# Optimization experiments

Hardware: AMD Instinct MI355X
Metric: run time of the kernel (lower is better)

## Reference

```python
import jax, jax.numpy as jnp
import numpy as np

B, S, D = 4, 4096, 2048
NUM_MODALITIES = 2


def setup_inputs() -> dict:
    key = jax.random.key(0)
    k_x, k_t, k_w0, k_b0, k_w1, k_b1 = jax.random.split(key, 6)
    scale = 1.0 / np.sqrt(D)
    return {
        "hidden_states": jax.random.normal(k_x, (B, S, D), dtype=jnp.float32),
        "type_ids": jax.random.randint(k_t, (B, S), 0, NUM_MODALITIES, dtype=jnp.int32),
        "W0": jax.random.uniform(k_w0, (D, D), jnp.float32, -scale, scale),
        "b0": jax.random.uniform(k_b0, (D,), jnp.float32, -scale, scale),
        "W1": jax.random.uniform(k_w1, (D, D), jnp.float32, -scale, scale),
        "b1": jax.random.uniform(k_b1, (D,), jnp.float32, -scale, scale),
    }


def reference(hidden_states, type_ids, W0, b0, W1, b1):
    # Original: gather tokens where type_ids == i, apply expert i's Linear,
    # scatter into a zero-init [B, S, out_dim] buffer. The masks partition
    # all tokens, so this equals a masked mixture of the two dense GEMMs.
    y0 = jnp.einsum("bsd,ed->bse", hidden_states, W0) + b0  # expert 0
    y1 = jnp.einsum("bsd,ed->bse", hidden_states, W1) + b1  # expert 1
    m0 = (type_ids == 0)[..., None]
    m1 = (type_ids == 1)[..., None]
    zero = jnp.zeros((), dtype=y0.dtype)
    return jnp.where(m0, y0, zero) + jnp.where(m1, y1, zero)
```

## Files before the change

### kernel.cpp

```cpp
#include <hip/hip_runtime.h>
#include <hip/hip_bf16.h>
#include <stdint.h>


#define T_TOK 16384
#define DDIM  2048
#define NT_K  32
#define MT    64
#define NTILE 8

typedef __attribute__((ext_vector_type(4))) float          f32x4;
typedef __attribute__((ext_vector_type(8))) short          bf16x8;
typedef __attribute__((ext_vector_type(2))) unsigned int   u32x2;

#define WS_HBF   0ull
#define WS_W0BF  67108864ull
#define WS_W1BF  75497472ull
#define WS_META  83886080ull
#define WS_IDX   83886208ull
#define WS_NEED  (WS_IDX + 65536ull)

__device__ __forceinline__ unsigned short cvt1_bf16(float f) {
  unsigned u = __builtin_bit_cast(unsigned, f);
  unsigned rnd = 0x7fffu + ((u >> 16) & 1u);
  return (unsigned short)((u + rnd) >> 16);
}

__device__ __forceinline__ void gload_lds16(const void* g, void* l) {
  __builtin_amdgcn_global_load_lds(
      (const __attribute__((address_space(1))) unsigned int*)g,
      (__attribute__((address_space(3))) unsigned int*)l, 16, 0, 0);
}

#define BAR()    asm volatile("s_barrier" ::: "memory")
#define VMCNT4() asm volatile("s_waitcnt vmcnt(4)" ::: "memory")
#define VMCNT0() asm volatile("s_waitcnt vmcnt(0)" ::: "memory")
#define LGKM0()  asm volatile("s_waitcnt lgkmcnt(0)" ::: "memory")

__global__ void k_prep(const float* __restrict__ H, const float* __restrict__ W0,
                       const float* __restrict__ W1, const int* __restrict__ typ,
                       unsigned short* __restrict__ Hbf,
                       unsigned short* __restrict__ W0bf,
                       unsigned short* __restrict__ W1bf,
                       int* __restrict__ meta) {
  const int gid = blockIdx.x * blockDim.x + threadIdx.x;
  if (gid < T_TOK && typ[gid] == 0) atomicAdd(&meta[0], 1);
  const int nH = T_TOK * DDIM / 4;
  const int nW = DDIM * DDIM / 4;
  const int total = nH + 2 * nW;
  const int stride = gridDim.x * blockDim.x;
  for (int i = gid; i < total; i += stride) {
    const float* s; unsigned short* d; int j;
    if (i < nH)           { s = H;  d = Hbf;  j = i; }
    else if (i < nH + nW) { s = W0; d = W0bf; j = i - nH; }
    else                  { s = W1; d = W1bf; j = i - nH - nW; }
    f32x4 v = ((const f32x4*)s)[j];
    unsigned p0 = (unsigned)cvt1_bf16(v[0]) | ((unsigned)cvt1_bf16(v[1]) << 16);
    unsigned p1 = (unsigned)cvt1_bf16(v[2]) | ((unsigned)cvt1_bf16(v[3]) << 16);
    u32x2 o; o[0] = p0; o[1] = p1;
    ((u32x2*)d)[j] = o;
  }
}

__global__ void k_scatter(const int* __restrict__ typ, int* __restrict__ meta,
                          int* __restrict__ idx) {
  int i = blockIdx.x * blockDim.x + threadIdx.x;
  if (i >= T_TOK) return;
  int c0 = meta[0];
  int t = typ[i];
  int pos = (t == 0) ? atomicAdd(&meta[2], 1) : c0 + atomicAdd(&meta[3], 1);
  idx[pos] = i;
}

__global__ __launch_bounds__(512, 2) void k_gemm256(
    const unsigned short* __restrict__ Hbf,
    const unsigned short* __restrict__ W0bf,
    const unsigned short* __restrict__ W1bf,
    const float* __restrict__ B0, const float* __restrict__ B1,
    const int* __restrict__ meta, const int* __restrict__ idx,
    float* __restrict__ OUT)
{
  __shared__ char lds[131072];

  const int orig = blockIdx.x;
  const int wg = (orig & 7) * 64 + (orig >> 3);
  const int my = wg >> 3;
  const int bx = wg & 7;

  const int tid  = threadIdx.x;
  const int lane = tid & 63;
  const int wid  = tid >> 6;
  const int wr   = wid >> 2;
  const int wc   = wid & 3;
  const int fr   = lane & 15;
  const int g    = lane >> 4;

  const int start = my * 256;
  const int c0    = meta[0];
  const int e0    = (start >= c0) ? 1 : 0;
  const int e1    = (start < c0 && c0 < start + 256) ? 1 : e0;
  const int colBase = bx * 256;

  const int cs = (lane & 3) ^ ((lane >> 3) & 3);
  const char* aS[2];
  int rt[2];
#pragma unroll
  for (int l = 0; l < 2; ++l) {
    int ch = 2 * wid + l;
    rt[l] = ch * 16 + (lane >> 2);
    int orow = idx[start + rt[l]];
    aS[l] = (const char*)Hbf + (size_t)orow * 4096 + cs * 16;
  }
  const int chB = (2 * wid) * 1024;

  const int sw = (g ^ ((fr >> 1) & 3)) << 4;
  int aF[8], bF[4];
#pragma unroll
  for (int m = 0; m < 8; ++m) aF[m] = ((wr * 128 + m * 16 + fr) << 6) + sw;
#pragma unroll
  for (int n = 0; n < 4; ++n) bF[n] = ((wc * 64 + n * 16 + fr) << 6) + sw;

  for (int e = e0; e <= e1; ++e) {
    const unsigned short* Wb = e ? W1bf : W0bf;
    const char* wS[2];
#pragma unroll
    for (int l = 0; l < 2; ++l)
      wS[l] = (const char*)(Wb + (size_t)(colBase + rt[l]) * DDIM) + cs * 16;

    f32x4 acc[8][4];
#pragma unroll
    for (int m = 0; m < 8; ++m)
#pragma unroll
      for (int n = 0; n < 4; ++n) acc[m][n] = (f32x4)0.0f;

    auto STAGE_A = [&](int d, int kh, int tn) {
      char* dst = lds + (d << 15) + (kh << 14) + chB;
      int ko = tn * 128 + kh * 64;
      gload_lds16(aS[0] + ko, dst);
      gload_lds16(aS[1] + ko, dst + 1024);
    };
    auto STAGE_B = [&](int d, int kh, int tn) {
      char* dst = lds + 65536 + (d << 15) + (kh << 14) + chB;
      int ko = tn * 128 + kh * 64;
      gload_lds16(wS[0] + ko, dst);
      gload_lds16(wS[1] + ko, dst + 1024);
    };

    VMCNT0();
    BAR();

    STAGE_A(0, 0, 0); STAGE_B(0, 0, 0); STAGE_A(0, 1, 0); STAGE_B(0, 1, 0);
    VMCNT4();
    BAR();

#pragma unroll 2
    for (int t = 0; t < NT_K; ++t) {
      const int c = t & 1, d = c ^ 1;
      int tn = t + 1; if (tn == NT_K) tn = NT_K - 1;
      const char* Ak0 = lds + (c << 15);
      const char* Ak1 = Ak0 + 16384;
      const char* Bk0 = lds + 65536 + (c << 15);
      const char* Bk1 = Bk0 + 16384;

      bf16x8 a[8], b0v, b1v, b2v, b3v;

#pragma unroll
      for (int m = 0; m < 8; ++m) a[m] = *(const bf16x8*)(Ak0 + aF[m]);
      b0v = *(const bf16x8*)(Bk0 + bF[0]);
      b1v = *(const bf16x8*)(Bk0 + bF[1]);
      STAGE_A(d, 0, tn);
      BAR(); LGKM0();
      __builtin_amdgcn_s_setprio(1);
#pragma unroll
      for (int m = 0; m < 8; ++m) {
        acc[m][0] = __builtin_amdgcn_mfma_f32_16x16x32_bf16(a[m], b0v, acc[m][0], 0, 0, 0);
        acc[m][1] = __builtin_amdgcn_mfma_f32_16x16x32_bf16(a[m], b1v, acc[m][1], 0, 0, 0);
      }
      __builtin_amdgcn_s_setprio(0);
      BAR();

      b2v = *(const bf16x8*)(Bk0 + bF[2]);
      b3v = *(const bf16x8*)(Bk0 + bF[3]);
      STAGE_B(d, 0, tn);
      VMCNT4();
      BAR(); LGKM0();
      __builtin_amdgcn_s_setprio(1);
#pragma unroll
      for (int m = 0; m < 8; ++m) {
        acc[m][2] = __builtin_amdgcn_mfma_f32_16x16x32_bf16(a[m], b2v, acc[m][2], 0, 0, 0);
        acc[m][3] = __builtin_amdgcn_mfma_f32_16x16x32_bf16(a[m], b3v, acc[m][3], 0, 0, 0);
      }
      __builtin_amdgcn_s_setprio(0);
      BAR();

#pragma unroll
      for (int m = 0; m < 8; ++m) a[m] = *(const bf16x8*)(Ak1 + aF[m]);
      b0v = *(const bf16x8*)(Bk1 + bF[0]);
      b1v = *(const bf16x8*)(Bk1 + bF[1]);
      STAGE_A(d, 1, tn);
      BAR(); LGKM0();
      __builtin_amdgcn_s_setprio(1);
#pragma unroll
      for (int m = 0; m < 8; ++m) {
        acc[m][0] = __builtin_amdgcn_mfma_f32_16x16x32_bf16(a[m], b0v, acc[m][0], 0, 0, 0);
        acc[m][1] = __builtin_amdgcn_mfma_f32_16x16x32_bf16(a[m], b1v, acc[m][1], 0, 0, 0);
      }
      __builtin_amdgcn_s_setprio(0);
      BAR();

      b2v = *(const bf16x8*)(Bk1 + bF[2]);
      b3v = *(const bf16x8*)(Bk1 + bF[3]);
      STAGE_B(d, 1, tn);
      VMCNT4();
      BAR(); LGKM0();
      __builtin_amdgcn_s_setprio(1);
#pragma unroll
      for (int m = 0; m < 8; ++m) {
        acc[m][2] = __builtin_amdgcn_mfma_f32_16x16x32_bf16(a[m], b2v, acc[m][2], 0, 0, 0);
        acc[m][3] = __builtin_amdgcn_mfma_f32_16x16x32_bf16(a[m], b3v, acc[m][3], 0, 0, 0);
      }
      __builtin_amdgcn_s_setprio(0);
      BAR();
    }

    const float* Bv = e ? B1 : B0;
    float bias[4];
    int cols[4];
#pragma unroll
    for (int n = 0; n < 4; ++n) {
      cols[n] = colBase + wc * 64 + n * 16 + fr;
      bias[n] = Bv[cols[n]];
    }
#pragma unroll
    for (int m = 0; m < 8; ++m) {
      int lb = wr * 128 + m * 16 + (g << 2);
#pragma unroll
      for (int j = 0; j < 4; ++j) {
        int p = start + lb + j;
        if (((p >= c0) ? 1 : 0) != e) continue;
        int orow = idx[p];
        float* op = OUT + (size_t)orow * DDIM;
#pragma unroll
        for (int n = 0; n < 4; ++n) op[cols[n]] = acc[m][n][j] + bias[n];
      }
    }
  }
}

#define BMd 64
#define BNd 64
#define BKd 32
#define LDW 36

__device__ __forceinline__ bf16x8 cvt_bf16x8(f32x4 lo, f32x4 hi) {
  bf16x8 r;
#pragma unroll
  for (int i = 0; i < 4; ++i) {
    r[i]     = (short)cvt1_bf16(lo[i]);
    r[i + 4] = (short)cvt1_bf16(hi[i]);
  }
  return r;
}

__global__ __launch_bounds__(256, 2) void mot_mfma_diag(
    const float* __restrict__ H,  const int* __restrict__ TYP,
    const float* __restrict__ W0, const float* __restrict__ B0,
    const float* __restrict__ W1, const float* __restrict__ B1,
    float* __restrict__ OUT)
{
  __shared__ float As[BMd * LDW];
  __shared__ float W0s[BNd * LDW];
  __shared__ float W1s[BNd * LDW];

  const int tid = threadIdx.x;
  const int rowBase = blockIdx.y * BMd;
  const int colBase = blockIdx.x * BNd;
  const int srow  = tid >> 3;
  const int scol4 = (tid & 7) << 2;
  const float* hA  = H  + (size_t)(rowBase + srow) * DDIM + scol4;
  const float* hW0 = W0 + (size_t)(colBase + srow) * DDIM + scol4;
  const float* hW1 = W1 + (size_t)(colBase + srow) * DDIM + scol4;

  const int lane = tid & 63;
  const int w    = tid >> 6;
  const int fr   = lane & 15;
  const int g    = lane >> 4;

  f32x4 acc0[4], acc1[4];
#pragma unroll
  for (int m = 0; m < 4; ++m) { acc0[m] = (f32x4)0.0f; acc1[m] = (f32x4)0.0f; }

  for (int k0 = 0; k0 < DDIM; k0 += BKd) {
    f32x4 va[2], v0[2], v1[2];
#pragma unroll
    for (int p = 0; p < 2; ++p) {
      va[p] = *(const f32x4*)(hA  + (size_t)p * 32 * DDIM);
      v0[p] = *(const f32x4*)(hW0 + (size_t)p * 32 * DDIM);
      v1[p] = *(const f32x4*)(hW1 + (size_t)p * 32 * DDIM);
    }
    hA += BKd; hW0 += BKd; hW1 += BKd;
    __syncthreads();
#pragma unroll
    for (int p = 0; p < 2; ++p) {
      int r = srow + 32 * p;
      *(f32x4*)(&As [r * LDW + scol4]) = va[p];
      *(f32x4*)(&W0s[r * LDW + scol4]) = v0[p];
      *(f32x4*)(&W1s[r * LDW + scol4]) = v1[p];
    }
    __syncthreads();

    bf16x8 af[4];
#pragma unroll
    for (int m = 0; m < 4; ++m) {
      const float* ap = &As[(m * 16 + fr) * LDW + g * 8];
      af[m] = cvt_bf16x8(*(const f32x4*)ap, *(const f32x4*)(ap + 4));
    }
    const float* b0p = &W0s[(w * 16 + fr) * LDW + g * 8];
    const float* b1p = &W1s[(w * 16 + fr) * LDW + g * 8];
    bf16x8 bf0 = cvt_bf16x8(*(const f32x4*)b0p, *(const f32x4*)(b0p + 4));
    bf16x8 bf1 = cvt_bf16x8(*(const f32x4*)b1p, *(const f32x4*)(b1p + 4));
#pragma unroll
    for (int m = 0; m < 4; ++m) {
      acc0[m] = __builtin_amdgcn_mfma_f32_16x16x32_bf16(af[m], bf0, acc0[m], 0, 0, 0);
      acc1[m] = __builtin_amdgcn_mfma_f32_16x16x32_bf16(af[m], bf1, acc1[m], 0, 0, 0);
    }
  }

  const int col = colBase + w * 16 + fr;
  const float bz0 = B0[col];
  const float bz1 = B1[col];
#pragma unroll
  for (int m = 0; m < 4; ++m)
#pragma unroll
    for (int j = 0; j < 4; ++j) {
      int row = rowBase + m * 16 + (g << 2) + j;
      int t = TYP[row];
      OUT[(size_t)row * DDIM + col] = (t == 0) ? (acc0[m][j] + bz0) : (acc1[m][j] + bz1);
    }
}

extern "C" void kernel_launch(void* const* d_in, const int* in_sizes, int n_in,
                              void* d_out, int out_size, void* d_ws, size_t ws_size,
                              hipStream_t stream) {
  const float* H   = (const float*)d_in[0];
  const int*   TYP = (const int*)  d_in[1];
  const float* W0  = (const float*)d_in[2];
  const float* B0v = (const float*)d_in[3];
  const float* W1  = (const float*)d_in[4];
  const float* B1v = (const float*)d_in[5];
  float* OUT = (float*)d_out;

  if (ws_size < WS_NEED) {
    dim3 grid(DDIM / BNd, T_TOK / BMd);
    mot_mfma_diag<<<grid, dim3(256), 0, stream>>>(H, TYP, W0, B0v, W1, B1v, OUT);
    return;
  }

  unsigned short* Hbf  = (unsigned short*)((char*)d_ws + WS_HBF);
  unsigned short* W0bf = (unsigned short*)((char*)d_ws + WS_W0BF);
  unsigned short* W1bf = (unsigned short*)((char*)d_ws + WS_W1BF);
  int* meta = (int*)((char*)d_ws + WS_META);
  int* idx  = (int*)((char*)d_ws + WS_IDX);

  hipMemsetAsync(meta, 0, 16, stream);
  k_prep   <<<4096, 256, 0, stream>>>(H, W0, W1, TYP, Hbf, W0bf, W1bf, meta);
  k_scatter<<<64,   256, 0, stream>>>(TYP, meta, idx);
  k_gemm256<<<MT * NTILE, 512, 0, stream>>>(Hbf, W0bf, W1bf, B0v, B1v, meta, idx, OUT);
}
```

Baseline: 238.0 us.

## Deepen GEMM prefetch pipeline and schedule mixed-expert row tile first

The main loop now prefetches global-to-LDS loads two k-steps ahead instead of one, reusing freed half-buffers within the current slot, and relaxes the vmcnt waits to allow more loads in flight. The per-phase register tiling moves from 8 A-fragments x 2 B-fragments to 4 A x 4 B, which changes how fragments are reused. The row tile that straddles the expert boundary (and needs both experts) is swapped into block slot zero so the heavier tile starts early. This aims to hide memory latency and reduce tail imbalance, at the cost of more complex buffer-reuse ordering that must stay race-free.

```diff
diff --git a/kernel.cpp b/kernel.cpp
--- a/kernel.cpp
+++ b/kernel.cpp
@@ -32,10 +32,10 @@
       (__attribute__((address_space(3))) unsigned int*)l, 16, 0, 0);
 }
 
-#define BAR()    asm volatile("s_barrier" ::: "memory")
-#define VMCNT4() asm volatile("s_waitcnt vmcnt(4)" ::: "memory")
-#define VMCNT0() asm volatile("s_waitcnt vmcnt(0)" ::: "memory")
-#define LGKM0()  asm volatile("s_waitcnt lgkmcnt(0)" ::: "memory")
+#define BAR()     asm volatile("s_barrier" ::: "memory")
+#define VMCNT10() asm volatile("s_waitcnt vmcnt(10)" ::: "memory")
+#define VMCNT0()  asm volatile("s_waitcnt vmcnt(0)" ::: "memory")
+#define LGKM0()   asm volatile("s_waitcnt lgkmcnt(0)" ::: "memory")
 
 __global__ void k_prep(const float* __restrict__ H, const float* __restrict__ W0,
                        const float* __restrict__ W1, const int* __restrict__ typ,
@@ -84,8 +84,12 @@
 
   const int orig = blockIdx.x;
   const int wg = (orig & 7) * 64 + (orig >> 3);
-  const int my = wg >> 3;
+  int my = wg >> 3;
   const int bx = wg & 7;
+
+  const int c0 = meta[0];
+  int ms = c0 >> 8; if (ms > MT - 1) ms = MT - 1;
+  my = (my == 0) ? ms : (my == ms) ? 0 : my;
 
   const int tid  = threadIdx.x;
   const int lane = tid & 63;
@@ -96,7 +100,6 @@
   const int g    = lane >> 4;
 
   const int start = my * 256;
-  const int c0    = meta[0];
   const int e0    = (start >= c0) ? 1 : 0;
   const int e1    = (start < c0 && c0 < start + 256) ? 1 : e0;
   const int colBase = bx * 256;
@@ -149,76 +152,80 @@
     VMCNT0();
     BAR();
 
-    STAGE_A(0, 0, 0); STAGE_B(0, 0, 0); STAGE_A(0, 1, 0); STAGE_B(0, 1, 0);
-    VMCNT4();
+    STAGE_B(0, 0, 0); STAGE_A(0, 0, 0);
+    STAGE_B(0, 1, 0); STAGE_A(0, 1, 0);
+    STAGE_B(1, 0, 1); STAGE_A(1, 0, 1);
+    STAGE_B(1, 1, 1);
+    VMCNT10();
     BAR();
 
 #pragma unroll 2
     for (int t = 0; t < NT_K; ++t) {
       const int c = t & 1, d = c ^ 1;
-      int tn = t + 1; if (tn == NT_K) tn = NT_K - 1;
+      int t1 = t + 1; if (t1 >= NT_K) t1 = NT_K - 1;
+      int t2 = t + 2; if (t2 >= NT_K) t2 = NT_K - 1;
       const char* Ak0 = lds + (c << 15);
       const char* Ak1 = Ak0 + 16384;
       const char* Bk0 = lds + 65536 + (c << 15);
       const char* Bk1 = Bk0 + 16384;
 
-      bf16x8 a[8], b0v, b1v, b2v, b3v;
-
-#pragma unroll
-      for (int m = 0; m < 8; ++m) a[m] = *(const bf16x8*)(Ak0 + aF[m]);
-      b0v = *(const bf16x8*)(Bk0 + bF[0]);
-      b1v = *(const bf16x8*)(Bk0 + bF[1]);
-      STAGE_A(d, 0, tn);
+      bf16x8 a[4], b[4];
+
+#pragma unroll
+      for (int m = 0; m < 4; ++m) a[m] = *(const bf16x8*)(Ak0 + aF[m]);
+#pragma unroll
+      for (int n = 0; n < 4; ++n) b[n] = *(const bf16x8*)(Bk0 + bF[n]);
+      STAGE_A(d, 1, t1);
       BAR(); LGKM0();
       __builtin_amdgcn_s_setprio(1);
 #pragma unroll
-      for (int m = 0; m < 8; ++m) {
-        acc[m][0] = __builtin_amdgcn_mfma_f32_16x16x32_bf16(a[m], b0v, acc[m][0], 0, 0, 0);
-        acc[m][1] = __builtin_amdgcn_mfma_f32_16x16x32_bf16(a[m], b1v, acc[m][1], 0, 0, 0);
-      }
+      for (int n = 0; n < 4; ++n)
+#pragma unroll
+        for (int m = 0; m < 4; ++m)
+          acc[m][n] = __builtin_amdgcn_mfma_f32_16x16x32_bf16(a[m], b[n], acc[m][n], 0, 0, 0);
       __builtin_amdgcn_s_setprio(0);
       BAR();
 
-      b2v = *(const bf16x8*)(Bk0 + bF[2]);
-      b3v = *(const bf16x8*)(Bk0 + bF[3]);
-      STAGE_B(d, 0, tn);
-      VMCNT4();
+#pragma unroll
+      for (int m = 0; m < 4; ++m) a[m] = *(const bf16x8*)(Ak0 + aF[m + 4]);
+      STAGE_B(c, 0, t2);
+      VMCNT10();
       BAR(); LGKM0();
       __builtin_amdgcn_s_setprio(1);
 #pragma unroll
-      for (int m = 0; m < 8; ++m) {
-        acc[m][2] = __builtin_amdgcn_mfma_f32_16x16x32_bf16(a[m], b2v, acc[m][2], 0, 0, 0);
-        acc[m][3] = __builtin_amdgcn_mfma_f32_16x16x32_bf16(a[m], b3v, acc[m][3], 0, 0, 0);
-      }
+      for (int n = 0; n < 4; ++n)
+#pragma unroll
+        for (int m = 0; m < 4; ++m)
+          acc[m + 4][n] = __builtin_amdgcn_mfma_f32_16x16x32_bf16(a[m], b[n], acc[m + 4][n], 0, 0, 0);
       __builtin_amdgcn_s_setprio(0);
       BAR();
 
 #pragma unroll
-      for (int m = 0; m < 8; ++m) a[m] = *(const bf16x8*)(Ak1 + aF[m]);
-      b0v = *(const bf16x8*)(Bk1 + bF[0]);
-      b1v = *(const bf16x8*)(Bk1 + bF[1]);
-      STAGE_A(d, 1, tn);
+      for (int m = 0; m < 4; ++m) a[m] = *(const bf16x8*)(Ak1 + aF[m]);
+#pragma unroll
+      for (int n = 0; n < 4; ++n) b[n] = *(const bf16x8*)(Bk1 + bF[n]);
+      STAGE_A(c, 0, t2);
       BAR(); LGKM0();
       __builtin_amdgcn_s_setprio(1);
 #pragma unroll
-      for (int m = 0; m < 8; ++m) {
-        acc[m][0] = __builtin_amdgcn_mfma_f32_16x16x32_bf16(a[m], b0v, acc[m][0], 0, 0, 0);
-        acc[m][1] = __builtin_amdgcn_mfma_f32_16x16x32_bf16(a[m], b1v, acc[m][1], 0, 0, 0);
-      }
+      for (int n = 0; n < 4; ++n)
+#pragma unroll
+        for (int m = 0; m < 4; ++m)
+          acc[m][n] = __builtin_amdgcn_mfma_f32_16x16x32_bf16(a[m], b[n], acc[m][n], 0, 0, 0);
       __builtin_amdgcn_s_setprio(0);
       BAR();
 
-      b2v = *(const bf16x8*)(Bk1 + bF[2]);
-      b3v = *(const bf16x8*)(Bk1 + bF[3]);
-      STAGE_B(d, 1, tn);
-      VMCNT4();
+#pragma unroll
+      for (int m = 0; m < 4; ++m) a[m] = *(const bf16x8*)(Ak1 + aF[m + 4]);
+      STAGE_B(c, 1, t2);
+      VMCNT10();
       BAR(); LGKM0();
       __builtin_amdgcn_s_setprio(1);
 #pragma unroll
-      for (int m = 0; m < 8; ++m) {
-        acc[m][2] = __builtin_amdgcn_mfma_f32_16x16x32_bf16(a[m], b2v, acc[m][2], 0, 0, 0);
-        acc[m][3] = __builtin_amdgcn_mfma_f32_16x16x32_bf16(a[m], b3v, acc[m][3], 0, 0, 0);
-      }
+      for (int n = 0; n < 4; ++n)
+#pragma unroll
+        for (int m = 0; m < 4; ++m)
+          acc[m + 4][n] = __builtin_amdgcn_mfma_f32_16x16x32_bf16(a[m], b[n], acc[m + 4][n], 0, 0, 0);
       __builtin_amdgcn_s_setprio(0);
       BAR();
     }
```

Result: no change. 238.0 us (-0.0%).

## Shrink GEMM tile to 256x128 with single-buffered LDS and remap boundary tile

Applied to the files above, without the earlier changes.

Changes the expert GEMM tile from 256x256 to 256x128 (1024 workgroups), uses a single-buffered 48KB LDS layout in place of the double-buffered 128KB one, and raises launch bounds to 4 waves-groups per CU. It also swaps the row-tile containing the expert boundary with tile 0 so the workgroup that runs both experts is scheduled first. The intent is higher occupancy and better load balance across CUs, at the cost of lower arithmetic intensity per tile and tighter load/compute overlap within the single buffer.

```diff
diff --git a/kernel.cpp b/kernel.cpp
--- a/kernel.cpp
+++ b/kernel.cpp
@@ -7,7 +7,7 @@
 #define DDIM  2048
 #define NT_K  32
 #define MT    64
-#define NTILE 8
+#define NTIL  16
 
 typedef __attribute__((ext_vector_type(4))) float          f32x4;
 typedef __attribute__((ext_vector_type(8))) short          bf16x8;
@@ -33,7 +33,7 @@
 }
 
 #define BAR()    asm volatile("s_barrier" ::: "memory")
-#define VMCNT4() asm volatile("s_waitcnt vmcnt(4)" ::: "memory")
+#define VMCNT1() asm volatile("s_waitcnt vmcnt(1)" ::: "memory")
 #define VMCNT0() asm volatile("s_waitcnt vmcnt(0)" ::: "memory")
 #define LGKM0()  asm volatile("s_waitcnt lgkmcnt(0)" ::: "memory")
 
@@ -72,7 +72,7 @@
   idx[pos] = i;
 }
 
-__global__ __launch_bounds__(512, 2) void k_gemm256(
+__global__ __launch_bounds__(512, 4) void k_gemm(
     const unsigned short* __restrict__ Hbf,
     const unsigned short* __restrict__ W0bf,
     const unsigned short* __restrict__ W1bf,
@@ -80,148 +80,147 @@
     const int* __restrict__ meta, const int* __restrict__ idx,
     float* __restrict__ OUT)
 {
-  __shared__ char lds[131072];
+  __shared__ char lds[49152];
 
   const int orig = blockIdx.x;
-  const int wg = (orig & 7) * 64 + (orig >> 3);
-  const int my = wg >> 3;
-  const int bx = wg & 7;
+  const int wg = (orig & 7) * 128 + (orig >> 3);
+  int my = wg >> 4;
+  const int bx = wg & 15;
+
+  const int c0 = meta[0];
+  int ms = c0 >> 8; if (ms > MT - 1) ms = MT - 1;
+  my = (my == 0) ? ms : (my == ms) ? 0 : my;
 
   const int tid  = threadIdx.x;
   const int lane = tid & 63;
   const int wid  = tid >> 6;
-  const int wr   = wid >> 2;
-  const int wc   = wid & 3;
+  const int wr   = wid >> 1;
+  const int wc   = wid & 1;
   const int fr   = lane & 15;
   const int g    = lane >> 4;
 
   const int start = my * 256;
-  const int c0    = meta[0];
   const int e0    = (start >= c0) ? 1 : 0;
   const int e1    = (start < c0 && c0 < start + 256) ? 1 : e0;
-  const int colBase = bx * 256;
+  const int colBase = bx * 128;
 
   const int cs = (lane & 3) ^ ((lane >> 3) & 3);
   const char* aS[2];
-  int rt[2];
 #pragma unroll
   for (int l = 0; l < 2; ++l) {
-    int ch = 2 * wid + l;
-    rt[l] = ch * 16 + (lane >> 2);
-    int orow = idx[start + rt[l]];
+    int r_tile = (2 * wid + l) * 16 + (lane >> 2);
+    int orow = idx[start + r_tile];
     aS[l] = (const char*)Hbf + (size_t)orow * 4096 + cs * 16;
   }
-  const int chB = (2 * wid) * 1024;
+  const int rb = wid * 16 + (lane >> 2);
+  const int chA = (2 * wid) * 1024;
+  const int chBb = wid * 1024;
 
   const int sw = (g ^ ((fr >> 1) & 3)) << 4;
-  int aF[8], bF[4];
-#pragma unroll
-  for (int m = 0; m < 8; ++m) aF[m] = ((wr * 128 + m * 16 + fr) << 6) + sw;
+  int aF[4], bF[4];
+#pragma unroll
+  for (int m = 0; m < 4; ++m) aF[m] = ((wr * 64 + m * 16 + fr) << 6) + sw;
 #pragma unroll
   for (int n = 0; n < 4; ++n) bF[n] = ((wc * 64 + n * 16 + fr) << 6) + sw;
+
+  char* const A0s = lds;
+  char* const A1s = lds + 16384;
+  char* const B0s = lds + 32768;
+  char* const B1s = lds + 40960;
 
   for (int e = e0; e <= e1; ++e) {
     const unsigned short* Wb = e ? W1bf : W0bf;
-    const char* wS[2];
-#pragma unroll
-    for (int l = 0; l < 2; ++l)
-      wS[l] = (const char*)(Wb + (size_t)(colBase + rt[l]) * DDIM) + cs * 16;
-
-    f32x4 acc[8][4];
-#pragma unroll
-    for (int m = 0; m < 8; ++m)
+    const char* wS = (const char*)(Wb + (size_t)(colBase + rb) * DDIM) + cs * 16;
+
+    f32x4 acc[4][4];
+#pragma unroll
+    for (int m = 0; m < 4; ++m)
 #pragma unroll
       for (int n = 0; n < 4; ++n) acc[m][n] = (f32x4)0.0f;
 
-    auto STAGE_A = [&](int d, int kh, int tn) {
-      char* dst = lds + (d << 15) + (kh << 14) + chB;
+    auto STAGE_A = [&](int kh, int tn) {
+      char* dst = lds + (kh << 14) + chA;
       int ko = tn * 128 + kh * 64;
       gload_lds16(aS[0] + ko, dst);
       gload_lds16(aS[1] + ko, dst + 1024);
     };
-    auto STAGE_B = [&](int d, int kh, int tn) {
-      char* dst = lds + 65536 + (d << 15) + (kh << 14) + chB;
-      int ko = tn * 128 + kh * 64;
-      gload_lds16(wS[0] + ko, dst);
-      gload_lds16(wS[1] + ko, dst + 1024);
+    auto STAGE_B = [&](int kh, int tn) {
+      char* dst = lds + 32768 + (kh << 13) + chBb;
+      gload_lds16(wS + tn * 128 + kh * 64, dst);
     };
 
     VMCNT0();
     BAR();
 
-    STAGE_A(0, 0, 0); STAGE_B(0, 0, 0); STAGE_A(0, 1, 0); STAGE_B(0, 1, 0);
-    VMCNT4();
+    STAGE_A(0, 0); STAGE_B(0, 0); STAGE_B(1, 0);
+    VMCNT1();
     BAR();
 
 #pragma unroll 2
     for (int t = 0; t < NT_K; ++t) {
-      const int c = t & 1, d = c ^ 1;
-      int tn = t + 1; if (tn == NT_K) tn = NT_K - 1;
-      const char* Ak0 = lds + (c << 15);
-      const char* Ak1 = Ak0 + 16384;
-      const char* Bk0 = lds + 65536 + (c << 15);
-      const char* Bk1 = Bk0 + 16384;
-
-      bf16x8 a[8], b0v, b1v, b2v, b3v;
-
-#pragma unroll
-      for (int m = 0; m < 8; ++m) a[m] = *(const bf16x8*)(Ak0 + aF[m]);
-      b0v = *(const bf16x8*)(Bk0 + bF[0]);
-      b1v = *(const bf16x8*)(Bk0 + bF[1]);
-      STAGE_A(d, 0, tn);
+      int t1 = t + 1; if (t1 == NT_K) t1 = NT_K - 1;
+      bf16x8 a0, a1, a2, a3, b[4];
+
+      a0 = *(const bf16x8*)(A0s + aF[0]);
+      a1 = *(const bf16x8*)(A0s + aF[1]);
+#pragma unroll
+      for (int n = 0; n < 4; ++n) b[n] = *(const bf16x8*)(B0s + bF[n]);
+      STAGE_A(1, t);
       BAR(); LGKM0();
       __builtin_amdgcn_s_setprio(1);
 #pragma unroll
-      for (int m = 0; m < 8; ++m) {
-        acc[m][0] = __builtin_amdgcn_mfma_f32_16x16x32_bf16(a[m], b0v, acc[m][0], 0, 0, 0);
-        acc[m][1] = __builtin_amdgcn_mfma_f32_16x16x32_bf16(a[m], b1v, acc[m][1], 0, 0, 0);
+      for (int n = 0; n < 4; ++n) {
+        acc[0][n] = __builtin_amdgcn_mfma_f32_16x16x32_bf16(a0, b[n], acc[0][n], 0, 0, 0);
+        acc[1][n] = __builtin_amdgcn_mfma_f32_16x16x32_bf16(a1, b[n], acc[1][n], 0, 0, 0);
       }
       __builtin_amdgcn_s_setprio(0);
       BAR();
 
-      b2v = *(const bf16x8*)(Bk0 + bF[2]);
-      b3v = *(const bf16x8*)(Bk0 + bF[3]);
-      STAGE_B(d, 0, tn);
-      VMCNT4();
+      a2 = *(const bf16x8*)(A0s + aF[2]);
+      a3 = *(const bf16x8*)(A0s + aF[3]);
+      STAGE_B(0, t1);
+      VMCNT1();
       BAR(); LGKM0();
       __builtin_amdgcn_s_setprio(1);
 #pragma unroll
-      for (int m = 0; m < 8; ++m) {
-        acc[m][2] = __builtin_amdgcn_mfma_f32_16x16x32_bf16(a[m], b2v, acc[m][2], 0, 0, 0);
-        acc[m][3] = __builtin_amdgcn_mfma_f32_16x16x32_bf16(a[m], b3v, acc[m][3], 0, 0, 0);
+      for (int n = 0; n < 4; ++n) {
+        acc[2][n] = __builtin_amdgcn_mfma_f32_16x16x32_bf16(a2, b[n], acc[2][n], 0, 0, 0);
+        acc[3][n] = __builtin_amdgcn_mfma_f32_16x16x32_bf16(a3, b[n], acc[3][n], 0, 0, 0);
       }
       __builtin_amdgcn_s_setprio(0);
       BAR();
 
-#pragma unroll
-      for (int m = 0; m < 8; ++m) a[m] = *(const bf16x8*)(Ak1 + aF[m]);
-      b0v = *(const bf16x8*)(Bk1 + bF[0]);
-      b1v = *(const bf16x8*)(Bk1 + bF[1]);
-      STAGE_A(d, 1, tn);
+      a0 = *(const bf16x8*)(A1s + aF[0]);
+      a1 = *(const bf16x8*)(A1s + aF[1]);
+#pragma unroll
+      for (int n = 0; n < 4; ++n) b[n] = *(const bf16x8*)(B1s + bF[n]);
+      STAGE_A(0, t1);
       BAR(); LGKM0();
       __builtin_amdgcn_s_setprio(1);
 #pragma unroll
-      for (int m = 0; m < 8; ++m) {
-        acc[m][0] = __builtin_amdgcn_mfma_f32_16x16x32_bf16(a[m], b0v, acc[m][0], 0, 0, 0);
-        acc[m][1] = __builtin_amdgcn_mfma_f32_16x16x32_bf16(a[m], b1v, acc[m][1], 0, 0, 0);
+      for (int n = 0; n < 4; ++n) {
+        acc[0][n] = __builtin_amdgcn_mfma_f32_16x16x32_bf16(a0, b[n], acc[0][n], 0, 0, 0);
+        acc[1][n] = __builtin_amdgcn_mfma_f32_16x16x32_bf16(a1, b[n], acc[1][n], 0, 0, 0);
       }
       __builtin_amdgcn_s_setprio(0);
       BAR();
 
-      b2v = *(const bf16x8*)(Bk1 + bF[2]);
-      b3v = *(const bf16x8*)(Bk1 + bF[3]);
-      STAGE_B(d, 1, tn);
-      VMCNT4();
+      a2 = *(const bf16x8*)(A1s + aF[2]);
+      a3 = *(const bf16x8*)(A1s + aF[3]);
+      STAGE_B(1, t1);
+      VMCNT1();
       BAR(); LGKM0();
       __builtin_amdgcn_s_setprio(1);
 #pragma unroll
-      for (int m = 0; m < 8; ++m) {
-        acc[m][2] = __builtin_amdgcn_mfma_f32_16x16x32_bf16(a[m], b2v, acc[m][2], 0, 0, 0);
-        acc[m][3] = __builtin_amdgcn_mfma_f32_16x16x32_bf16(a[m], b3v, acc[m][3], 0, 0, 0);
+      for (int n = 0; n < 4; ++n) {
+        acc[2][n] = __builtin_amdgcn_mfma_f32_16x16x32_bf16(a2, b[n], acc[2][n], 0, 0, 0);
+        acc[3][n] = __builtin_amdgcn_mfma_f32_16x16x32_bf16(a3, b[n], acc[3][n], 0, 0, 0);
       }
       __builtin_amdgcn_s_setprio(0);
       BAR();
     }
+
+    VMCNT0();
 
     const float* Bv = e ? B1 : B0;
     float bias[4];
@@ -232,8 +231,8 @@
       bias[n] = Bv[cols[n]];
     }
 #pragma unroll
-    for (int m = 0; m < 8; ++m) {
-      int lb = wr * 128 + m * 16 + (g << 2);
+    for (int m = 0; m < 4; ++m) {
+      int lb = wr * 64 + m * 16 + (g << 2);
 #pragma unroll
       for (int j = 0; j < 4; ++j) {
         int p = start + lb + j;
@@ -365,5 +364,5 @@
   hipMemsetAsync(meta, 0, 16, stream);
   k_prep   <<<4096, 256, 0, stream>>>(H, W0, W1, TYP, Hbf, W0bf, W1bf, meta);
   k_scatter<<<64,   256, 0, stream>>>(TYP, meta, idx);
-  k_gemm256<<<MT * NTILE, 512, 0, stream>>>(Hbf, W0bf, W1bf, B0v, B1v, meta, idx, OUT);
-}
+  k_gemm<<<MT * NTIL, 512, 0, stream>>>(Hbf, W0bf, W1bf, B0v, B1v, meta, idx, OUT);
+}
```

Result: slower. 253.0 us (+6.3%).
